# Performance work log

Measured on AMD Instinct MI355X. Metric: run time of the kernel, lower is better.

## Reference

```python
import jax, jax.numpy as jnp
import numpy as np

B, T, D, H = 4, 2048, 1024, 4
DK = D // H      # head_k_dim = 256
DV = D // H      # head_v_dim = 256
M = DK           # num_slots defaults to head_k_dim
GATE_NORM = 16.0
CLAMP_MIN, CLAMP_MAX = -32.0, 32.0
EPS = 1e-5
ROPE_BASE = 10000.0


def setup_inputs() -> dict:
    key = jax.random.key(0)
    ks = jax.random.split(key, 8)
    sd = 0.02  # stands in for xavier_uniform with gain 2**-2.5
    return {
        "hidden_states": jax.random.normal(ks[0], (B, T, D), jnp.float32),
        "q_w": jax.random.normal(ks[1], (D, D), jnp.float32) * sd,
        "k_w": jax.random.normal(ks[2], (D, D), jnp.float32) * sd,
        "v_w": jax.random.normal(ks[3], (D, D), jnp.float32) * sd,
        "g_w": jax.random.normal(ks[4], (D, D), jnp.float32) * sd,
        "s_w": jax.random.normal(ks[5], (D, H * M), jnp.float32) * sd,
        "sg_w": jax.random.normal(ks[6], (D, H), jnp.float32) * sd,
        "gn_w": jnp.ones((DV,), jnp.float32),
        "o_w": jax.random.normal(ks[7], (D, D), jnp.float32) * sd,
    }


def _rope(x):
    # x: [B, T, H, DK]; non-interleaved (flash-attn style) rotary, full head dim
    half = x.shape[-1] // 2
    inv = 1.0 / (ROPE_BASE ** (jnp.arange(half, dtype=jnp.float32) / half))
    ang = jnp.arange(x.shape[1], dtype=jnp.float32)[:, None] * inv[None, :]  # [T, half]
    cos = jnp.cos(ang)[None, :, None, :]
    sin = jnp.sin(ang)[None, :, None, :]
    x1, x2 = x[..., :half], x[..., half:]
    return jnp.concatenate([x1 * cos - x2 * sin, x2 * cos + x1 * sin], -1)


def _abc(q, k, v, s):
    # ABC linear attention with slot memory (fla chunk_abc semantics, g=None path).
    # q, k: [B,H,T,DK]; v: [B,H,T,DV]; s: [B,H,T,M] (clamped slot logits)
    scale = q.shape[-1] ** -0.5
    z = jax.lax.cumlogsumexp(s, axis=2)                    # running log-normalizer
    s_n = jnp.exp(s - z)                                   # normalized slot write weights
    g = jnp.exp(jnp.concatenate([z[:, :, :1], z[:, :, :-1]], 2) - z)  # per-step decay in (0,1]

    tm = lambda x: jnp.moveaxis(x, 2, 0)                   # time-major for scan

    # stage 1: key memory  hk[B,H,DK,M];  ok_t = scale * q_t @ hk_t
    def step_k(hk, inp):
        q_t, k_t, s_t, g_t = inp
        hk = hk * g_t[:, :, None, :] + k_t[..., None] * s_t[:, :, None, :]
        return hk, jnp.einsum('bhk,bhkm->bhm', q_t, hk)
    hk0 = jnp.zeros(q.shape[:2] + (q.shape[-1], s.shape[-1]), q.dtype)
    _, ok = jax.lax.scan(step_k, hk0, (tm(q * scale), tm(k), tm(s_n), tm(g)))

    qv = jax.nn.softmax(ok, axis=-1)                       # slot read weights, [T,B,H,M]

    # stage 2: value memory  hv[B,H,M,DV];  ov_t = qv_t @ hv_t
    def step_v(hv, inp):
        qv_t, v_t, s_t, g_t = inp
        hv = hv * g_t[..., None] + s_t[..., None] * v_t[:, :, None, :]
        return hv, jnp.einsum('bhm,bhmv->bhv', qv_t, hv)
    hv0 = jnp.zeros(v.shape[:2] + (s.shape[-1], v.shape[-1]), v.dtype)
    _, ov = jax.lax.scan(step_v, hv0, (qv, tm(v), tm(s_n), tm(g)))
    return jnp.moveaxis(ov, 0, 2)                          # [B,H,T,DV]


def reference(hidden_states, q_w, k_w, v_w, g_w, s_w, sg_w, gn_w, o_w):
    x = hidden_states
    q = (x @ q_w).reshape(B, T, H, DK)
    k = (x @ k_w).reshape(B, T, H, DK)
    v = (x @ v_w).reshape(B, T, H, DV).transpose(0, 2, 1, 3)       # [B,H,T,DV]
    q, k = _rope(q), _rope(k)
    q = q.transpose(0, 2, 1, 3)                                    # [B,H,T,DK]
    k = k.transpose(0, 2, 1, 3)

    s = (x @ s_w).reshape(B, T, H, M).transpose(0, 2, 1, 3)        # [B,H,T,M]
    s = jnp.clip(s, CLAMP_MIN, CLAMP_MAX)

    sg = jax.nn.log_sigmoid(x @ sg_w).transpose(0, 2, 1) / GATE_NORM  # [B,H,T]
    k = k * jnp.exp(jnp.cumsum(sg, axis=2))[..., None]

    o = _abc(q, k, v, s).transpose(0, 2, 1, 3)                     # [B,T,H,DV]

    g = (x @ g_w).reshape(B, T, H, DV)
    rms = o * jax.lax.rsqrt(jnp.mean(o * o, axis=-1, keepdims=True) + EPS) * gn_w
    o = (rms * g * jax.nn.sigmoid(g)).reshape(B, T, D)             # RMSNorm + swish gate
    return o @ o_w
```

## Files before the change

### kernel.cpp

```cpp
#include <hip/hip_runtime.h>
#include <hip/hip_bf16.h>
#include <stdint.h>
#include <stddef.h>
#include <math.h>

typedef __bf16 bf8_t __attribute__((ext_vector_type(8)));
typedef __bf16 bf4_t __attribute__((ext_vector_type(4)));
typedef float  f4_t  __attribute__((ext_vector_type(4)));
typedef unsigned int u32;

#define DEV static __device__ __forceinline__

namespace abc {
constexpr int B = 4, T = 2048, D = 1024, H = 4;
constexpr int BT = B * T;
constexpr int CH = 64;
constexpr int NC = T / CH;
constexpr int BH = B * H;
constexpr float SCALE = 0.0625f;
constexpr float GN = 16.0f;
constexpr float EPS = 1e-5f;
}

DEV f4_t mfma16(bf8_t a, bf8_t b, f4_t c) {
  return __builtin_amdgcn_mfma_f32_16x16x32_bf16(a, b, c, 0, 0, 0);
}

DEV void glds16(const void* g, void* l) {
  __builtin_amdgcn_global_load_lds(
      (const __attribute__((address_space(1))) u32*)g,
      (__attribute__((address_space(3))) u32*)l, 16, 0, 0);
}

__global__ __launch_bounds__(256)
void cvt_x_kernel(const float* __restrict__ x, __bf16* __restrict__ xb)
{
  const int idx = blockIdx.x * 256 + threadIdx.x;
  const float4* src = reinterpret_cast<const float4*>(x);
  float4 a = src[(size_t)idx * 2];
  float4 b = src[(size_t)idx * 2 + 1];
  bf8_t o;
  o[0] = (__bf16)a.x; o[1] = (__bf16)a.y; o[2] = (__bf16)a.z; o[3] = (__bf16)a.w;
  o[4] = (__bf16)b.x; o[5] = (__bf16)b.y; o[6] = (__bf16)b.z; o[7] = (__bf16)b.w;
  reinterpret_cast<bf8_t*>(xb)[idx] = o;
}

__global__ __launch_bounds__(256)
void cvt_w_kernel(const float* __restrict__ w0, const float* __restrict__ w1,
                  const float* __restrict__ w2, const float* __restrict__ w3,
                  const float* __restrict__ w4, const float* __restrict__ w5,
                  __bf16* __restrict__ wt)
{
  const int z = blockIdx.z;
  const float* W = (z == 0) ? w0 : (z == 1) ? w1 : (z == 2) ? w2
                 : (z == 3) ? w3 : (z == 4) ? w4 : w5;
  const int n0 = blockIdx.x * 64, k0 = blockIdx.y * 64;
  __shared__ __bf16 Ts[64][72];
  const int tid = threadIdx.x;
  #pragma unroll
  for (int i = 0; i < 4; i++) {
    int p = tid + 256 * i;
    int row = p >> 4, c4 = p & 15;
    float4 v = *reinterpret_cast<const float4*>(W + (size_t)(k0 + row) * 1024 + n0 + c4 * 4);
    Ts[c4 * 4 + 0][row] = (__bf16)v.x;
    Ts[c4 * 4 + 1][row] = (__bf16)v.y;
    Ts[c4 * 4 + 2][row] = (__bf16)v.z;
    Ts[c4 * 4 + 3][row] = (__bf16)v.w;
  }
  __syncthreads();
  #pragma unroll
  for (int i = 0; i < 2; i++) {
    int p = tid + 256 * i;
    int n = p >> 3, kq = p & 7;
    bf8_t o = *reinterpret_cast<const bf8_t*>(&Ts[n][kq * 8]);
    *reinterpret_cast<bf8_t*>(wt + (size_t)z * 1024 * 1024 + (size_t)(n0 + n) * 1024 + k0 + kq * 8) = o;
  }
}

template<bool OUT_BF16>
__global__ __launch_bounds__(256)
void gemm_bt_kernel(const __bf16* __restrict__ A, const __bf16* __restrict__ BtB,
                    void* __restrict__ Cp)
{
  using namespace abc;
  constexpr int K = 1024;
  const int z = blockIdx.z;
  const __bf16* Bt = BtB + (size_t)z * K * 1024;
  const int n0 = blockIdx.x * 128;
  const int m0 = blockIdx.y * 128;
  __shared__ __bf16 As[128 * 64];
  __shared__ __bf16 Bs[128 * 64];
  const int tid = threadIdx.x;
  const int lane = tid & 63, wvid = tid >> 6;
  const int wr = wvid >> 1, wc = wvid & 1;
  const int quad = lane >> 4, l16 = lane & 15;
  const f4_t fzero = {0.f, 0.f, 0.f, 0.f};
  f4_t acc[4][4];
  #pragma unroll
  for (int i = 0; i < 4; i++)
    #pragma unroll
    for (int j = 0; j < 4; j++) acc[i][j] = fzero;

  const int chunk_row = tid >> 3;
  const int chunk_col = tid & 7;
  for (int k0 = 0; k0 < K; k0 += 64) {
    __syncthreads();
    #pragma unroll
    for (int i = 0; i < 4; i++) {
      glds16(A + (size_t)(m0 + i * 32 + chunk_row) * K + k0 + chunk_col * 8,
             &As[(size_t)(i * 256 + wvid * 64) * 8]);
    }
    #pragma unroll
    for (int i = 0; i < 4; i++) {
      glds16(Bt + (size_t)(n0 + i * 32 + chunk_row) * K + k0 + chunk_col * 8,
             &Bs[(size_t)(i * 256 + wvid * 64) * 8]);
    }
    __syncthreads();
    #pragma unroll
    for (int ks = 0; ks < 2; ks++) {
      bf8_t af[4], bfv[4];
      #pragma unroll
      for (int i = 0; i < 4; i++)
        af[i] = *reinterpret_cast<const bf8_t*>(
            &As[(size_t)(wr * 64 + i * 16 + l16) * 64 + ks * 32 + quad * 8]);
      #pragma unroll
      for (int j = 0; j < 4; j++)
        bfv[j] = *reinterpret_cast<const bf8_t*>(
            &Bs[(size_t)(wc * 64 + j * 16 + l16) * 64 + ks * 32 + quad * 8]);
      #pragma unroll
      for (int i = 0; i < 4; i++)
        #pragma unroll
        for (int j = 0; j < 4; j++)
          acc[i][j] = mfma16(af[i], bfv[j], acc[i][j]);
    }
  }
  const int crow = m0 + wr * 64, ccol = n0 + wc * 64;
  if (OUT_BF16) {
    __bf16* C = (__bf16*)Cp + (size_t)z * BT * 1024;
    #pragma unroll
    for (int i = 0; i < 4; i++)
      #pragma unroll
      for (int j = 0; j < 4; j++)
        #pragma unroll
        for (int r = 0; r < 4; r++)
          C[(size_t)(crow + i * 16 + quad * 4 + r) * 1024 + ccol + j * 16 + l16] =
              (__bf16)acc[i][j][r];
  } else {
    float* C = (float*)Cp;
    #pragma unroll
    for (int i = 0; i < 4; i++)
      #pragma unroll
      for (int j = 0; j < 4; j++)
        #pragma unroll
        for (int r = 0; r < 4; r++)
          C[(size_t)(crow + i * 16 + quad * 4 + r) * 1024 + ccol + j * 16 + l16] =
              acc[i][j][r];
  }
}

__global__ __launch_bounds__(256)
void sg_kernel(const float* __restrict__ x, const float* __restrict__ sgw,
               float* __restrict__ sgl)
{
  using namespace abc;
  const int wvid = threadIdx.x >> 6, lane = threadIdx.x & 63;
  const int bt = blockIdx.x * 4 + wvid;
  const float* xr = x + (size_t)bt * 1024;
  float a0 = 0, a1 = 0, a2 = 0, a3 = 0;
  #pragma unroll 4
  for (int u = 0; u < 16; u++) {
    int i = u * 64 + lane;
    float xv = xr[i];
    float4 w = *reinterpret_cast<const float4*>(sgw + (size_t)i * 4);
    a0 += xv * w.x; a1 += xv * w.y; a2 += xv * w.z; a3 += xv * w.w;
  }
  #pragma unroll
  for (int off = 32; off > 0; off >>= 1) {
    a0 += __shfl_down(a0, off);
    a1 += __shfl_down(a1, off);
    a2 += __shfl_down(a2, off);
    a3 += __shfl_down(a3, off);
  }
  if (lane == 0) {
    const int b = bt >> 11, t = bt & (T - 1);
    float r[4] = {a0, a1, a2, a3};
    #pragma unroll
    for (int h = 0; h < 4; h++) {
      float v = r[h];
      float ls = fminf(v, 0.f) - log1pf(expf(-fabsf(v)));
      sgl[(size_t)(b * 4 + h) * T + t] = ls * (1.0f / GN);
    }
  }
}

__global__ __launch_bounds__(256)
void scan_kernel(const float* __restrict__ sgl, float* __restrict__ sgc)
{
  using namespace abc;
  const int bh = blockIdx.x;
  const float* in = sgl + (size_t)bh * T;
  float* out = sgc + (size_t)bh * T;
  __shared__ float part[256];
  const int tid = threadIdx.x;
  float v[8]; float s = 0.f;
  #pragma unroll
  for (int i = 0; i < 8; i++) { v[i] = in[tid * 8 + i]; s += v[i]; }
  part[tid] = s;
  __syncthreads();
  for (int off = 1; off < 256; off <<= 1) {
    float a = (tid >= off) ? part[tid - off] : 0.f;
    __syncthreads();
    part[tid] += a;
    __syncthreads();
  }
  float run = (tid > 0) ? part[tid - 1] : 0.f;
  #pragma unroll
  for (int i = 0; i < 8; i++) { run += v[i]; out[tid * 8 + i] = run; }
}

__global__ __launch_bounds__(256)
void prep_kernel(__bf16* __restrict__ q, __bf16* __restrict__ k,
                 __bf16* __restrict__ s, const float* __restrict__ sgc)
{
  using namespace abc;
  const int bt = blockIdx.x;
  const int b = bt >> 11, t = bt & (T - 1);
  const int tid = threadIdx.x;
  const size_t ro = (size_t)bt * 1024;
  #pragma unroll
  for (int i = 0; i < 2; i++) {
    int p = tid + 256 * i;
    int h = p >> 7, d = p & 127;
    float inv = expf(-(float)d * (9.210340371976184f / 128.0f));
    float ang = (float)t * inv;
    float sn, cs;
    sincosf(ang, &sn, &cs);
    size_t base = ro + (size_t)h * 256 + d;
    float q1 = (float)q[base], q2 = (float)q[base + 128];
    q[base]       = (__bf16)(q1 * cs - q2 * sn);
    q[base + 128] = (__bf16)(q2 * cs + q1 * sn);
    float dec = expf(sgc[(size_t)(b * 4 + h) * T + t]);
    float k1 = (float)k[base], k2 = (float)k[base + 128];
    k[base]       = (__bf16)((k1 * cs - k2 * sn) * dec);
    k[base + 128] = (__bf16)((k2 * cs + k1 * sn) * dec);
  }
  #pragma unroll
  for (int i = 0; i < 4; i++) {
    int e = tid + 256 * i;
    float v = (float)s[ro + e];
    v = fminf(fmaxf(v, -32.f), 32.f);
    s[ro + e] = (__bf16)expf(v);
  }
}

__global__ __launch_bounds__(256)
void transpose_kernel(const __bf16* __restrict__ s0, const __bf16* __restrict__ s1,
                      __bf16* __restrict__ d0, __bf16* __restrict__ d1)
{
  using namespace abc;
  const int c = blockIdx.x, bh = blockIdx.y, z = blockIdx.z;
  const int b = bh >> 2, h = bh & 3;
  const size_t R = (size_t)b * T + (size_t)c * CH;
  const int F = h * 256;
  const __bf16* src = z ? s1 : s0;
  __bf16* dst = (z ? d1 : d0) + ((size_t)bh * NC + c) * (256 * 64);
  __shared__ __bf16 L[256 * 64];
  const int tid = threadIdx.x;
  #pragma unroll
  for (int j = 0; j < 8; j++) {
    int p = tid + 256 * j;
    int t = p >> 5, fc = p & 31;
    bf8_t v = *reinterpret_cast<const bf8_t*>(src + (R + t) * 1024 + F + fc * 8);
    const int sw = ((t >> 3) ^ (fc & 7)) * 8 + (t & 7);
    #pragma unroll
    for (int u = 0; u < 8; u++)
      L[(fc * 8 + u) * 64 + sw] = v[u];
  }
  __syncthreads();
  #pragma unroll
  for (int j = 0; j < 8; j++) {
    int p = tid + 256 * j;
    int f = p >> 3, q = p & 7;
    int phys = q ^ ((f >> 3) & 7);
    bf8_t o = *reinterpret_cast<const bf8_t*>(&L[f * 64 + phys * 8]);
    *reinterpret_cast<bf8_t*>(dst + (size_t)f * 64 + q * 8) = o;
  }
}

__global__ __launch_bounds__(256)
void chunkstate_kernel(const __bf16* __restrict__ KT, const __bf16* __restrict__ VT,
                       const __bf16* __restrict__ AT,
                       __bf16* __restrict__ HKc, __bf16* __restrict__ HVc,
                       float* __restrict__ csA)
{
  using namespace abc;
  const int c = blockIdx.x, bh = blockIdx.y, part = blockIdx.z;
  const size_t TB = ((size_t)bh * NC + c) * (256 * 64);
  const bool isHV = part >= 2;
  const int p2 = part & 1;
  const __bf16* Aop = (isHV ? VT : AT) + TB;
  const __bf16* Bop = (isHV ? AT : KT) + TB;
  const int tid = threadIdx.x;
  if (part == 2) {
    float ssum = 0.f;
    #pragma unroll
    for (int u = 0; u < 8; u++) {
      bf8_t v = *reinterpret_cast<const bf8_t*>(AT + TB + (size_t)tid * 64 + u * 8);
      #pragma unroll
      for (int w = 0; w < 8; w++) ssum += (float)v[w];
    }
    csA[((size_t)bh * NC + c) * 256 + tid] = ssum;
  }
  const int lane = tid & 63, wvid = tid >> 6;
  const int quad = lane >> 4, l16 = lane & 15;
  const int row0 = p2 * 128 + wvid * 32;
  const f4_t fzero = {0.f, 0.f, 0.f, 0.f};
  f4_t acc[2][16];
  #pragma unroll
  for (int a = 0; a < 2; a++)
    #pragma unroll
    for (int ct = 0; ct < 16; ct++) acc[a][ct] = fzero;
  #pragma unroll
  for (int ks = 0; ks < 2; ks++) {
    bf8_t af0 = *reinterpret_cast<const bf8_t*>(Aop + (size_t)(row0 + l16) * 64 + ks * 32 + quad * 8);
    bf8_t af1 = *reinterpret_cast<const bf8_t*>(Aop + (size_t)(row0 + 16 + l16) * 64 + ks * 32 + quad * 8);
    #pragma unroll
    for (int ct = 0; ct < 16; ct++) {
      bf8_t bv = *reinterpret_cast<const bf8_t*>(Bop + (size_t)(ct * 16 + l16) * 64 + ks * 32 + quad * 8);
      acc[0][ct] = mfma16(af0, bv, acc[0][ct]);
      acc[1][ct] = mfma16(af1, bv, acc[1][ct]);
    }
  }
  __bf16* out = (isHV ? HVc : HKc) + ((size_t)bh * NC + c) * 65536;
  #pragma unroll
  for (int rt = 0; rt < 2; rt++)
    #pragma unroll
    for (int ct = 0; ct < 16; ct++)
      #pragma unroll
      for (int r = 0; r < 4; r++)
        out[(size_t)(row0 + rt * 16 + quad * 4 + r) * 256 + ct * 16 + l16] =
            (__bf16)acc[rt][ct][r];
}

__global__ __launch_bounds__(256)
void prefix_state_kernel(__bf16* __restrict__ HKc, __bf16* __restrict__ HVc)
{
  using namespace abc;
  const int bh = blockIdx.y;
  __bf16* base = (blockIdx.z ? HVc : HKc) + (size_t)bh * NC * 65536;
  const int e = (blockIdx.x * 256 + threadIdx.x) * 4;
  float run0 = 0, run1 = 0, run2 = 0, run3 = 0;
  for (int c = 0; c < NC; c++) {
    __bf16* p = base + (size_t)c * 65536 + e;
    bf4_t v = *reinterpret_cast<const bf4_t*>(p);
    bf4_t o;
    o[0] = (__bf16)run0; o[1] = (__bf16)run1; o[2] = (__bf16)run2; o[3] = (__bf16)run3;
    run0 += (float)v[0]; run1 += (float)v[1]; run2 += (float)v[2]; run3 += (float)v[3];
    *reinterpret_cast<bf4_t*>(p) = o;
  }
}

__global__ __launch_bounds__(256)
void prefix_csa_kernel(float* __restrict__ csA)
{
  using namespace abc;
  const int bh = blockIdx.x, m = threadIdx.x;
  float run = 0.f;
  for (int c = 0; c < NC; c++) {
    float* p = csA + ((size_t)bh * NC + c) * 256 + m;
    float v = *p; *p = run; run += v;
  }
}

__global__ __launch_bounds__(256)
void attn_kernel(const __bf16* __restrict__ qg, const __bf16* __restrict__ kg,
                 const __bf16* __restrict__ ag, const __bf16* __restrict__ gg,
                 const __bf16* __restrict__ ATp, const __bf16* __restrict__ VTp,
                 const __bf16* __restrict__ HKp, const __bf16* __restrict__ HVp,
                 const float* __restrict__ Zp, const float* __restrict__ gnw,
                 __bf16* __restrict__ yout)
{
  using namespace abc;
  const int c = blockIdx.x, bh = blockIdx.y;
  const int b = bh >> 2, h = bh & 3;
  const size_t R = (size_t)b * T + (size_t)c * CH;
  const int F = h * 256;
  const int tid = threadIdx.x;
  const int lane = tid & 63, wvid = tid >> 6;
  const int quad = lane >> 4, l16 = lane & 15;

  __shared__ __bf16 Ws[64][264];
  __shared__ __bf16 S1s[64][72];
  __shared__ float zs[256];
  __shared__ float gns[256];

  zs[tid] = Zp[((size_t)bh * NC + c) * 256 + tid];
  gns[tid] = gnw[tid];
  __syncthreads();

  const f4_t fzero = {0.f, 0.f, 0.f, 0.f};
  const __bf16* qrow = qg + (R + wvid * 16 + l16) * 1024 + F;

  f4_t s1a[4];
  #pragma unroll
  for (int it = 0; it < 4; it++) s1a[it] = fzero;
  #pragma unroll
  for (int ks = 0; ks < 8; ks++) {
    bf8_t aq = *reinterpret_cast<const bf8_t*>(qrow + ks * 32 + quad * 8);
    #pragma unroll
    for (int it = 0; it < 4; it++) {
      bf8_t bk = *reinterpret_cast<const bf8_t*>(
          kg + (R + it * 16 + l16) * 1024 + F + ks * 32 + quad * 8);
      s1a[it] = mfma16(aq, bk, s1a[it]);
    }
  }
  #pragma unroll
  for (int it = 0; it < 4; it++)
    #pragma unroll
    for (int r = 0; r < 4; r++) {
      int tl = wvid * 16 + quad * 4 + r;
      int il = it * 16 + l16;
      S1s[tl][il] = (il <= tl) ? (__bf16)s1a[it][r] : (__bf16)0.0f;
    }

  const __bf16* atb = ATp + ((size_t)bh * NC + c) * (256 * 64);
  f4_t aok[16], acum[16];
  #pragma unroll
  for (int mt = 0; mt < 16; mt++) { aok[mt] = fzero; acum[mt] = fzero; }
  #pragma unroll
  for (int iks = 0; iks < 2; iks++) {
    bf8_t s1f = *reinterpret_cast<const bf8_t*>(&S1s[wvid * 16 + l16][iks * 32 + quad * 8]);
    bf8_t lf;
    #pragma unroll
    for (int j = 0; j < 8; j++)
      lf[j] = (iks * 32 + quad * 8 + j <= wvid * 16 + l16) ? (__bf16)1.0f : (__bf16)0.0f;
    #pragma unroll
    for (int mt = 0; mt < 16; mt++) {
      bf8_t bfa = *reinterpret_cast<const bf8_t*>(
          atb + (size_t)(mt * 16 + l16) * 64 + iks * 32 + quad * 8);
      aok[mt]  = mfma16(s1f, bfa, aok[mt]);
      acum[mt] = mfma16(lf,  bfa, acum[mt]);
    }
  }
  const __bf16* hkb = HKp + ((size_t)bh * NC + c) * 65536;
  #pragma unroll
  for (int ks = 0; ks < 8; ks++) {
    bf8_t aq = *reinterpret_cast<const bf8_t*>(qrow + ks * 32 + quad * 8);
    #pragma unroll
    for (int mt = 0; mt < 16; mt++) {
      bf8_t bv = *reinterpret_cast<const bf8_t*>(
          hkb + (size_t)(mt * 16 + l16) * 256 + ks * 32 + quad * 8);
      aok[mt] = mfma16(aq, bv, aok[mt]);
    }
  }
  #pragma unroll
  for (int r = 0; r < 4; r++) {
    float ovv[16], sa[16];
    float mx = -3.0e38f;
    #pragma unroll
    for (int mt = 0; mt < 16; mt++) {
      sa[mt] = zs[mt * 16 + l16] + acum[mt][r];
      ovv[mt] = SCALE * aok[mt][r] / sa[mt];
      mx = fmaxf(mx, ovv[mt]);
    }
    #pragma unroll
    for (int off = 1; off < 16; off <<= 1) mx = fmaxf(mx, __shfl_xor(mx, off));
    float se = 0.f;
    #pragma unroll
    for (int mt = 0; mt < 16; mt++) { ovv[mt] = __expf(ovv[mt] - mx); se += ovv[mt]; }
    #pragma unroll
    for (int off = 1; off < 16; off <<= 1) se += __shfl_xor(se, off);
    float inv = 1.0f / se;
    int tl = wvid * 16 + quad * 4 + r;
    #pragma unroll
    for (int mt = 0; mt < 16; mt++)
      Ws[tl][mt * 16 + l16] = (__bf16)(ovv[mt] * inv / sa[mt]);
  }

  f4_t pacc[4];
  #pragma unroll
  for (int it = 0; it < 4; it++) pacc[it] = fzero;
  #pragma unroll
  for (int ks = 0; ks < 8; ks++) {
    bf8_t wf = *reinterpret_cast<const bf8_t*>(&Ws[wvid * 16 + l16][ks * 32 + quad * 8]);
    #pragma unroll
    for (int it = 0; it < 4; it++) {
      bf8_t ba = *reinterpret_cast<const bf8_t*>(
          ag + (R + it * 16 + l16) * 1024 + F + ks * 32 + quad * 8);
      pacc[it] = mfma16(wf, ba, pacc[it]);
    }
  }
  #pragma unroll
  for (int it = 0; it < 4; it++)
    #pragma unroll
    for (int r = 0; r < 4; r++) {
      int tl = wvid * 16 + quad * 4 + r;
      int il = it * 16 + l16;
      S1s[tl][il] = (il <= tl) ? (__bf16)pacc[it][r] : (__bf16)0.0f;
    }

  f4_t oacc[16];
  #pragma unroll
  for (int vt = 0; vt < 16; vt++) oacc[vt] = fzero;
  const __bf16* hvb = HVp + ((size_t)bh * NC + c) * 65536;
  #pragma unroll
  for (int ks = 0; ks < 8; ks++) {
    bf8_t wf = *reinterpret_cast<const bf8_t*>(&Ws[wvid * 16 + l16][ks * 32 + quad * 8]);
    #pragma unroll
    for (int vt = 0; vt < 16; vt++) {
      bf8_t bv = *reinterpret_cast<const bf8_t*>(
          hvb + (size_t)(vt * 16 + l16) * 256 + ks * 32 + quad * 8);
      oacc[vt] = mfma16(wf, bv, oacc[vt]);
    }
  }
  const __bf16* vtb = VTp + ((size_t)bh * NC + c) * (256 * 64);
  #pragma unroll
  for (int iks = 0; iks < 2; iks++) {
    bf8_t pf = *reinterpret_cast<const bf8_t*>(&S1s[wvid * 16 + l16][iks * 32 + quad * 8]);
    #pragma unroll
    for (int vt = 0; vt < 16; vt++) {
      bf8_t bvt = *reinterpret_cast<const bf8_t*>(
          vtb + (size_t)(vt * 16 + l16) * 64 + iks * 32 + quad * 8);
      oacc[vt] = mfma16(pf, bvt, oacc[vt]);
    }
  }
  #pragma unroll
  for (int r = 0; r < 4; r++) {
    float ss = 0.f;
    #pragma unroll
    for (int vt = 0; vt < 16; vt++) ss += oacc[vt][r] * oacc[vt][r];
    #pragma unroll
    for (int off = 1; off < 16; off <<= 1) ss += __shfl_xor(ss, off);
    float rinv = rsqrtf(ss * (1.0f / 256.0f) + EPS);
    int tl = wvid * 16 + quad * 4 + r;
    const __bf16* grow = gg + (R + tl) * 1024 + F;
    __bf16* yrow = yout + (R + tl) * 1024 + F;
    #pragma unroll
    for (int vt = 0; vt < 16; vt++) {
      int v = vt * 16 + l16;
      float gvl = (float)grow[v];
      float yv = oacc[vt][r] * rinv * gns[v] * gvl / (1.0f + __expf(-gvl));
      yrow[v] = (__bf16)yv;
    }
  }
}

extern "C" void kernel_launch(void* const* d_in, const int* in_sizes, int n_in,
                              void* d_out, int out_size, void* d_ws, size_t ws_size,
                              hipStream_t stream) {
  using namespace abc;
  (void)in_sizes; (void)n_in; (void)out_size; (void)ws_size;
  const float* x    = (const float*)d_in[0];
  const float* q_w  = (const float*)d_in[1];
  const float* k_w  = (const float*)d_in[2];
  const float* v_w  = (const float*)d_in[3];
  const float* g_w  = (const float*)d_in[4];
  const float* s_w  = (const float*)d_in[5];
  const float* sg_w = (const float*)d_in[6];
  const float* gn_w = (const float*)d_in[7];
  const float* o_w  = (const float*)d_in[8];
  float* out = (float*)d_out;

  char* ws = (char*)d_ws;
  const size_t PROJ = (size_t)BT * 1024;
  __bf16* proj = (__bf16*)ws;
  __bf16* q_bf = proj + 0 * PROJ;
  __bf16* k_bf = proj + 1 * PROJ;
  __bf16* v_bf = proj + 2 * PROJ;
  __bf16* g_bf = proj + 3 * PROJ;
  __bf16* a_bf = proj + 4 * PROJ;
  __bf16* xb   = proj + 5 * PROJ;
  float* sgl = (float*)(ws + (size_t)96 * 1024 * 1024);
  float* sgc = sgl + (size_t)BH * T;
  float* csA = sgc + (size_t)BH * T;
  __bf16* HKc = (__bf16*)(ws + (size_t)97 * 1024 * 1024);
  __bf16* HVc = HKc + (size_t)BH * NC * 65536;
  __bf16* wt  = (__bf16*)(ws + (size_t)225 * 1024 * 1024);
  __bf16* KT  = (__bf16*)(ws + (size_t)237 * 1024 * 1024);
  __bf16* VT  = xb;
  __bf16* AT  = v_bf;
  __bf16* y_bf = KT;

  dim3 blk(256);
  cvt_w_kernel<<<dim3(16, 16, 6), blk, 0, stream>>>(q_w, k_w, v_w, g_w, s_w, o_w, wt);
  cvt_x_kernel<<<dim3(BT * 1024 / (256 * 8)), blk, 0, stream>>>(x, xb);
  gemm_bt_kernel<true><<<dim3(8, 64, 5), blk, 0, stream>>>(xb, wt, proj);
  sg_kernel<<<dim3(BT / 4), blk, 0, stream>>>(x, sg_w, sgl);
  scan_kernel<<<dim3(BH), blk, 0, stream>>>(sgl, sgc);
  prep_kernel<<<dim3(BT), blk, 0, stream>>>(q_bf, k_bf, a_bf, sgc);
  transpose_kernel<<<dim3(NC, BH, 2), blk, 0, stream>>>(k_bf, v_bf, KT, VT);
  transpose_kernel<<<dim3(NC, BH, 1), blk, 0, stream>>>(a_bf, a_bf, AT, AT);
  chunkstate_kernel<<<dim3(NC, BH, 4), blk, 0, stream>>>(KT, VT, AT, HKc, HVc, csA);
  prefix_state_kernel<<<dim3(64, BH, 2), blk, 0, stream>>>(HKc, HVc);
  prefix_csa_kernel<<<dim3(BH), blk, 0, stream>>>(csA);
  attn_kernel<<<dim3(NC, BH), blk, 0, stream>>>(
      q_bf, k_bf, a_bf, g_bf, AT, VT, HKc, HVc, csA, gn_w, y_bf);
  gemm_bt_kernel<false><<<dim3(8, 64, 1), blk, 0, stream>>>(
      y_bf, wt + (size_t)5 * 1024 * 1024, out);
}
```

Before: 568.8 us.

## Double-buffer attn_kernel B-operands through swizzled LDS with async global_load_lds

```diff
diff --git a/kernel.cpp b/kernel.cpp
--- a/kernel.cpp
+++ b/kernel.cpp
@@ -30,6 +30,21 @@
   __builtin_amdgcn_global_load_lds(
       (const __attribute__((address_space(1))) u32*)g,
       (__attribute__((address_space(3))) u32*)l, 16, 0, 0);
+}
+
+template<int ROWS>
+DEV void stage(const __bf16* __restrict__ g, int S ,
+               __bf16* lds, int tid) {
+  #pragma unroll
+  for (int i = 0; i < ROWS / 64; i++) {
+    int p = i * 256 + tid;
+    int m = p >> 2;
+    int q = (p & 3) ^ (m & 3);
+    glds16(g + (size_t)m * S + q * 8, lds + (i * 256 + (tid & ~63)) * 8);
+  }
+}
+DEV bf8_t bfrag(const __bf16* sl, int m, int quad) {
+  return *reinterpret_cast<const bf8_t*>(sl + m * 32 + ((quad ^ (m & 3)) << 3));
 }
 
 __global__ __launch_bounds__(256)
@@ -389,30 +404,47 @@
   const int lane = tid & 63, wvid = tid >> 6;
   const int quad = lane >> 4, l16 = lane & 15;
 
+  __shared__ __bf16 ST[2][8192];
   __shared__ __bf16 Ws[64][264];
   __shared__ __bf16 S1s[64][72];
   __shared__ float zs[256];
   __shared__ float gns[256];
 
+  const __bf16* atb = ATp + ((size_t)bh * NC + c) * (256 * 64);
+  const __bf16* vtb = VTp + ((size_t)bh * NC + c) * (256 * 64);
+  const __bf16* hkb = HKp + ((size_t)bh * NC + c) * 65536;
+  const __bf16* hvb = HVp + ((size_t)bh * NC + c) * 65536;
+  const __bf16* kbase = kg + R * 1024 + F;
+  const __bf16* abase = ag + R * 1024 + F;
+
   zs[tid] = Zp[((size_t)bh * NC + c) * 256 + tid];
   gns[tid] = gnw[tid];
+
+  const __bf16* qrow = qg + (R + wvid * 16 + l16) * 1024 + F;
+  bf8_t aq[8];
+  #pragma unroll
+  for (int ks = 0; ks < 8; ks++)
+    aq[ks] = *reinterpret_cast<const bf8_t*>(qrow + ks * 32 + quad * 8);
+
+  const f4_t fzero = {0.f, 0.f, 0.f, 0.f};
+
+  stage<64>(kbase, 1024, ST[0], tid);
   __syncthreads();
 
-  const f4_t fzero = {0.f, 0.f, 0.f, 0.f};
-  const __bf16* qrow = qg + (R + wvid * 16 + l16) * 1024 + F;
-
   f4_t s1a[4];
   #pragma unroll
   for (int it = 0; it < 4; it++) s1a[it] = fzero;
   #pragma unroll
   for (int ks = 0; ks < 8; ks++) {
-    bf8_t aq = *reinterpret_cast<const bf8_t*>(qrow + ks * 32 + quad * 8);
+    if (ks < 7) stage<64>(kbase + (ks + 1) * 32, 1024, ST[(ks + 1) & 1], tid);
+    else        stage<256>(atb, 64, ST[0], tid);
+    const __bf16* sl = ST[ks & 1];
     #pragma unroll
     for (int it = 0; it < 4; it++) {
-      bf8_t bk = *reinterpret_cast<const bf8_t*>(
-          kg + (R + it * 16 + l16) * 1024 + F + ks * 32 + quad * 8);
-      s1a[it] = mfma16(aq, bk, s1a[it]);
-    }
+      bf8_t bk = bfrag(sl, it * 16 + l16, quad);
+      s1a[it] = mfma16(aq[ks], bk, s1a[it]);
+    }
+    __syncthreads();
   }
   #pragma unroll
   for (int it = 0; it < 4; it++)
@@ -423,12 +455,14 @@
       S1s[tl][il] = (il <= tl) ? (__bf16)s1a[it][r] : (__bf16)0.0f;
     }
 
-  const __bf16* atb = ATp + ((size_t)bh * NC + c) * (256 * 64);
   f4_t aok[16], acum[16];
   #pragma unroll
   for (int mt = 0; mt < 16; mt++) { aok[mt] = fzero; acum[mt] = fzero; }
   #pragma unroll
   for (int iks = 0; iks < 2; iks++) {
+    if (iks == 0) stage<256>(atb + 32, 64, ST[1], tid);
+    else          stage<256>(hkb, 256, ST[0], tid);
+    const __bf16* sl = ST[iks & 1];
     bf8_t s1f = *reinterpret_cast<const bf8_t*>(&S1s[wvid * 16 + l16][iks * 32 + quad * 8]);
     bf8_t lf;
     #pragma unroll
@@ -436,23 +470,26 @@
       lf[j] = (iks * 32 + quad * 8 + j <= wvid * 16 + l16) ? (__bf16)1.0f : (__bf16)0.0f;
     #pragma unroll
     for (int mt = 0; mt < 16; mt++) {
-      bf8_t bfa = *reinterpret_cast<const bf8_t*>(
-          atb + (size_t)(mt * 16 + l16) * 64 + iks * 32 + quad * 8);
+      bf8_t bfa = bfrag(sl, mt * 16 + l16, quad);
       aok[mt]  = mfma16(s1f, bfa, aok[mt]);
       acum[mt] = mfma16(lf,  bfa, acum[mt]);
     }
-  }
-  const __bf16* hkb = HKp + ((size_t)bh * NC + c) * 65536;
+    __syncthreads();
+  }
+
   #pragma unroll
   for (int ks = 0; ks < 8; ks++) {
-    bf8_t aq = *reinterpret_cast<const bf8_t*>(qrow + ks * 32 + quad * 8);
+    if (ks < 7) stage<256>(hkb + (ks + 1) * 32, 256, ST[(ks + 1) & 1], tid);
+    else        stage<64>(abase, 1024, ST[0], tid);
+    const __bf16* sl = ST[ks & 1];
     #pragma unroll
     for (int mt = 0; mt < 16; mt++) {
-      bf8_t bv = *reinterpret_cast<const bf8_t*>(
-          hkb + (size_t)(mt * 16 + l16) * 256 + ks * 32 + quad * 8);
-      aok[mt] = mfma16(aq, bv, aok[mt]);
-    }
-  }
+      bf8_t bv = bfrag(sl, mt * 16 + l16, quad);
+      aok[mt] = mfma16(aq[ks], bv, aok[mt]);
+    }
+    __syncthreads();
+  }
+
   #pragma unroll
   for (int r = 0; r < 4; r++) {
     float ovv[16], sa[16];
@@ -482,13 +519,16 @@
   for (int it = 0; it < 4; it++) pacc[it] = fzero;
   #pragma unroll
   for (int ks = 0; ks < 8; ks++) {
+    if (ks < 7) stage<64>(abase + (ks + 1) * 32, 1024, ST[(ks + 1) & 1], tid);
+    else        stage<256>(hvb, 256, ST[0], tid);
+    const __bf16* sl = ST[ks & 1];
     bf8_t wf = *reinterpret_cast<const bf8_t*>(&Ws[wvid * 16 + l16][ks * 32 + quad * 8]);
     #pragma unroll
     for (int it = 0; it < 4; it++) {
-      bf8_t ba = *reinterpret_cast<const bf8_t*>(
-          ag + (R + it * 16 + l16) * 1024 + F + ks * 32 + quad * 8);
+      bf8_t ba = bfrag(sl, it * 16 + l16, quad);
       pacc[it] = mfma16(wf, ba, pacc[it]);
     }
+    __syncthreads();
   }
   #pragma unroll
   for (int it = 0; it < 4; it++)
@@ -502,28 +542,32 @@
   f4_t oacc[16];
   #pragma unroll
   for (int vt = 0; vt < 16; vt++) oacc[vt] = fzero;
-  const __bf16* hvb = HVp + ((size_t)bh * NC + c) * 65536;
   #pragma unroll
   for (int ks = 0; ks < 8; ks++) {
+    if (ks < 7) stage<256>(hvb + (ks + 1) * 32, 256, ST[(ks + 1) & 1], tid);
+    else        stage<256>(vtb, 64, ST[0], tid);
+    const __bf16* sl = ST[ks & 1];
     bf8_t wf = *reinterpret_cast<const bf8_t*>(&Ws[wvid * 16 + l16][ks * 32 + quad * 8]);
     #pragma unroll
     for (int vt = 0; vt < 16; vt++) {
-      bf8_t bv = *reinterpret_cast<const bf8_t*>(
-          hvb + (size_t)(vt * 16 + l16) * 256 + ks * 32 + quad * 8);
+      bf8_t bv = bfrag(sl, vt * 16 + l16, quad);
       oacc[vt] = mfma16(wf, bv, oacc[vt]);
     }
-  }
-  const __bf16* vtb = VTp + ((size_t)bh * NC + c) * (256 * 64);
+    __syncthreads();
+  }
   #pragma unroll
   for (int iks = 0; iks < 2; iks++) {
+    if (iks == 0) stage<256>(vtb + 32, 64, ST[1], tid);
+    const __bf16* sl = ST[iks & 1];
     bf8_t pf = *reinterpret_cast<const bf8_t*>(&S1s[wvid * 16 + l16][iks * 32 + quad * 8]);
     #pragma unroll
     for (int vt = 0; vt < 16; vt++) {
-      bf8_t bvt = *reinterpret_cast<const bf8_t*>(
-          vtb + (size_t)(vt * 16 + l16) * 64 + iks * 32 + quad * 8);
+      bf8_t bvt = bfrag(sl, vt * 16 + l16, quad);
       oacc[vt] = mfma16(pf, bvt, oacc[vt]);
     }
-  }
+    __syncthreads();
+  }
+
   #pragma unroll
   for (int r = 0; r < 4; r++) {
     float ss = 0.f;
```

New measurement: 502.3 us. -11.7%, faster.
